# Kernel tuning notes

Hardware: AMD Instinct MI355X
Metric: run time of the kernel (lower is better)

Reference implementation:

```python
import jax, jax.numpy as jnp
import numpy as np

B = 8          # batch_size
N = 2048       # N_particles
D_SP = 2       # spatial dims
D = 16         # D_SP + hidden_dim
K = 32         # max_num_neighbors
R = 0.08       # neighbor_radius
DT = 0.01      # leapfrog step
BIG = 1e9


def setup_inputs() -> dict:
    key = jax.random.key(0)
    ks = jax.random.split(key, 8)
    H, C = 64, 32
    # node state: small random hidden features, deterministic disk positions
    x = jax.random.normal(ks[0], (B * N, D), dtype=jnp.float32) * 0.001
    i = jnp.arange(N, dtype=jnp.float32)
    golden = jnp.pi * (3.0 - jnp.sqrt(5.0))
    theta = i * golden
    r = 0.6 * jnp.sqrt((i + 0.5) / N)
    pos = jnp.stack([r * jnp.cos(theta), r * jnp.sin(theta)], axis=1)  # [N,2]
    pos = jnp.tile(pos, (B, 1)) + 0.01 * jax.random.normal(ks[1], (B * N, 2), dtype=jnp.float32)
    x = x.at[:, :D_SP].set(pos)
    W1 = jax.random.normal(ks[2], (2 * D, H), dtype=jnp.float32) * (1.0 / np.sqrt(2 * D))
    b1 = jnp.zeros((H,), jnp.float32)
    W2 = jax.random.normal(ks[3], (H, C), dtype=jnp.float32) * (1.0 / np.sqrt(H))
    b2 = jnp.zeros((C,), jnp.float32)
    Wout = jax.random.normal(ks[4], (C, 1), dtype=jnp.float32) * (1.0 / np.sqrt(C))
    bout = jnp.zeros((1,), jnp.float32)
    batch = jnp.repeat(jnp.arange(B, dtype=jnp.int64), N)
    return {"x": x, "W1": W1, "b1": b1, "W2": W2, "b2": b2,
            "Wout": Wout, "bout": bout, "batch": batch, "steps": 2}


def reference(x, W1, b1, W2, b2, Wout, bout, batch, steps):
    Bn, Df = x.shape
    Bc = int(np.asarray(batch)[-1]) + 1      # batch is contiguous blocks
    Nn = Bn // Bc
    eye = jnp.eye(Nn, dtype=x.dtype) * BIG   # no self-loops (loop=False)

    def hamiltonian(xv):
        xb = xv.reshape(Bc, Nn, Df)
        pos = xb[:, :, :D_SP]                              # [B,N,2]
        # radius_graph: pairwise sq-dist per simulation, capped at K neighbors
        d2 = jnp.sum((pos[:, :, None, :] - pos[:, None, :, :]) ** 2, axis=-1)  # [B,N,N]
        d2 = d2 + eye
        negd, idx = jax.lax.top_k(-d2, K)                  # K nearest per node
        valid = (-negd) < (R * R)                          # [B,N,K]
        # gather neighbor states (HNNConv message on concat(x_i, x_j))
        xj = xb[jnp.arange(Bc)[:, None, None], idx]        # [B,N,K,D]
        xi = jnp.broadcast_to(xb[:, :, None, :], xj.shape)
        m = jnp.tanh(jnp.concatenate([xi, xj], axis=-1) @ W1 + b1)  # [B,N,K,H]
        m = m @ W2 + b2                                    # [B,N,K,C]
        m = jnp.where(valid[..., None], m, 0.0)
        agg = m.sum(axis=2)                                # sum aggregation [B,N,C]
        h = agg @ Wout + bout                              # per-node Hamiltonian [B,N,1]
        return h.sum()

    for _ in range(int(steps)):
        dHdx = jax.grad(hamiltonian)(x)
        x = x - DT * dHdx
    return x
```

## Files before the change

kernel.cpp:

```cpp
#include <hip/hip_runtime.h>
#include <cstdint>
#include <cstddef>

#define BB   8
#define NN   2048
#define DD   16
#define HHH  64
#define KK   32
#define CAP  96
#define FCAP 48
#define DT_C 0.01f
#define R2_C (0.08f * 0.08f)

#define GRID 17
#define NCEL (GRID * GRID)
#define GOFF 0.68f
#define CINV 12.5f
#define CSTRIDE 320

#define WPB   8
#define BLOCK (WPB * 64)

__device__ __forceinline__ float dist2(float px, float py, float qx, float qy) {
    float dx = __fsub_rn(px, qx);
    float dy = __fsub_rn(py, qy);
    return __fadd_rn(__fmul_rn(dx, dx), __fmul_rn(dy, dy));
}

__device__ __forceinline__ float dtanh_xla(float zz) {
    float xx = fminf(fmaxf(zz, -9.f), 9.f);
    float x2 = xx * xx;
    float p = fmaf(x2, -2.76076847742355e-16f, 2.00018790482477e-13f);
    p = fmaf(x2, p, -8.60467152213735e-11f);
    p = fmaf(x2, p, 5.12229709037114e-08f);
    p = fmaf(x2, p, 1.48572235717979e-05f);
    p = fmaf(x2, p, 6.37261928875436e-04f);
    p = fmaf(x2, p, 4.89352455891786e-03f);
    p = xx * p;
    float q = fmaf(x2, 1.19825839466702e-06f, 1.18534705686654e-04f);
    q = fmaf(x2, q, 2.26843463243900e-03f);
    q = fmaf(x2, q, 4.89352518554385e-03f);
    float r = __builtin_amdgcn_rcpf(q);
    float t = p * r;
    t = fmaf(fmaf(-q, t, p), r, t);
    return fmaf(-t, t, 1.0f);
}

__device__ __forceinline__ int prefix_cnt(unsigned long long m) {
    return (int)__builtin_amdgcn_mbcnt_hi(
        (unsigned)(m >> 32), __builtin_amdgcn_mbcnt_lo((unsigned)m, 0u));
}

__device__ __forceinline__ int swizzled_slot(int blk, int w, int& bbase) {
    bbase = (blk & 7) << 11;
    return (blk >> 3) * WPB + w;
}

__device__ __forceinline__ int clampi(int v, int lo, int hi) {
    return v < lo ? lo : (v > hi ? hi : v);
}

struct Win { int rs0, rl0, rs1, rl1, rs2, rl2, tot; };
__device__ __forceinline__ Win cell_window(const int* CS, float px, float py) {
    Win W;
    int cx = clampi((int)((px + GOFF) * CINV), 0, GRID - 1);
    int cy = clampi((int)((py + GOFF) * CINV), 0, GRID - 1);
    int xlo = cx > 0 ? cx - 1 : 0;
    int xhi = cx < GRID - 1 ? cx + 1 : GRID - 1;
    W.rs0 = 0; W.rl0 = 0; W.rs2 = 0; W.rl2 = 0;
    if (cy > 0) {
        int a = CS[(cy - 1) * GRID + xlo], b = CS[(cy - 1) * GRID + xhi + 1];
        W.rs0 = a; W.rl0 = b - a;
    }
    {
        int a = CS[cy * GRID + xlo], b = CS[cy * GRID + xhi + 1];
        W.rs1 = a; W.rl1 = b - a;
    }
    if (cy < GRID - 1) {
        int a = CS[(cy + 1) * GRID + xlo], b = CS[(cy + 1) * GRID + xhi + 1];
        W.rs2 = a; W.rl2 = b - a;
    }
    W.tot = W.rl0 + W.rl1 + W.rl2;
    return W;
}
__device__ __forceinline__ int win_map(const Win& W, int t) {
    int j = W.rs0 + t;
    int u1 = t - W.rl0;
    if (u1 >= 0) j = W.rs1 + u1;
    int u2 = u1 - W.rl1;
    if (u2 >= 0) j = W.rs2 + u2;
    return j;
}

template <bool FIRST>
__global__ __launch_bounds__(1024) void k_bin(
    const float* __restrict__ x, const float* __restrict__ pos,
    const float* __restrict__ W2, const float* __restrict__ Wout,
    float2* __restrict__ sortedPos, unsigned short* __restrict__ sortedIdx,
    int* __restrict__ cellStart, float* __restrict__ vOut) {
    __shared__ int hist[NCEL], base[NCEL + 1], cursor[NCEL];
    int bat = blockIdx.x, bbase = bat << 11, tid = threadIdx.x;
    if (tid < NCEL) hist[tid] = 0;
    if (blockIdx.x == 0 && tid >= 512 && tid < 512 + HHH) {
        int hh = tid - 512;
        float acc = 0.f;
        for (int c = 0; c < 32; c++) acc = fmaf(W2[hh * 32 + c], Wout[c], acc);
        vOut[hh] = acc;
    }
    __syncthreads();
    float2 q[2]; int cid[2];
#pragma unroll
    for (int u = 0; u < 2; ++u) {
        int i = tid + (u << 10);
        float2 qq = FIRST ? *(const float2*)(x + (size_t)(bbase + i) * DD)
                          : *(const float2*)(pos + (size_t)(bbase + i) * 2);
        q[u] = qq;
        int cx = clampi((int)((qq.x + GOFF) * CINV), 0, GRID - 1);
        int cy = clampi((int)((qq.y + GOFF) * CINV), 0, GRID - 1);
        cid[u] = cy * GRID + cx;
        atomicAdd(&hist[cid[u]], 1);
    }
    __syncthreads();
    if (tid < 64) {
        int loc[5], s = 0;
#pragma unroll
        for (int k = 0; k < 5; ++k) {
            int idx = tid * 5 + k;
            loc[k] = (idx < NCEL) ? hist[idx] : 0;
            s += loc[k];
        }
        int pre = s;
#pragma unroll
        for (int off = 1; off < 64; off <<= 1) {
            int t = __shfl_up(pre, off);
            if (tid >= off) pre += t;
        }
        pre -= s;
#pragma unroll
        for (int k = 0; k < 5; ++k) {
            int idx = tid * 5 + k;
            if (idx <= NCEL) base[idx] = pre;
            pre += loc[k];
        }
    }
    __syncthreads();
    if (tid < NCEL) cursor[tid] = base[tid];
    if (tid <= NCEL) cellStart[bat * CSTRIDE + tid] = base[tid];
    __syncthreads();
#pragma unroll
    for (int u = 0; u < 2; ++u) {
        int dst = atomicAdd(&cursor[cid[u]], 1);
        sortedPos[bbase + dst] = q[u];
        sortedIdx[bbase + dst] = (unsigned short)(tid + (u << 10));
    }
}

__global__ __launch_bounds__(BLOCK, 4) void k_cut(
    const float* __restrict__ x,
    const float2* __restrict__ sortedPos, const unsigned short* __restrict__ sortedIdx,
    const int* __restrict__ cellStart, const float* __restrict__ W1,
    float* __restrict__ cutArr,
    float* __restrict__ Asp, float* __restrict__ Dsp) {
    __shared__ float sD[WPB][CAP];

    int tid = threadIdx.x;
    int w = tid >> 6, lane = tid & 63;
    int bbase;
    int s = swizzled_slot(blockIdx.x, w, bbase);
    int bat = bbase >> 11;
    int gs = bbase + s;

    int jol = (int)sortedIdx[gs];
    const float* xrow = x + (size_t)(bbase + jol) * DD;
    float xv = (lane < DD) ? xrow[lane] : 0.f;
    float px = __shfl(xv, 0), py = __shfl(xv, 1);
    double A = 0.0, Dv = 0.0;
#pragma unroll
    for (int f = 0; f < DD; f++) {
        float xf = __shfl(xv, f);
        A  = fma((double)xf, (double)W1[f * HHH + lane], A);
        Dv = fma((double)xf, (double)W1[(DD + f) * HHH + lane], Dv);
    }
    Asp[((size_t)gs << 6) + lane] = (float)A;
    Dsp[((size_t)gs << 6) + lane] = (float)Dv;

    const int* CS = cellStart + bat * CSTRIDE;
    Win W = cell_window(CS, px, py);
    int cnt = 0;
    for (int c0 = 0; c0 < W.tot; c0 += 64) {
        int t = c0 + lane;
        int j = win_map(W, t);
        bool in = t < W.tot;
        float2 q = sortedPos[bbase + (in ? j : 0)];
        float d2 = dist2(px, py, q.x, q.y);
        bool hit = in && (d2 < R2_C);
        unsigned long long m = __ballot(hit);
        int idx = cnt + prefix_cnt(m);
        if (hit && idx < CAP) sD[w][idx] = d2;
        cnt += (int)__popcll(m);
    }
    if (cnt > CAP) cnt = CAP;
    __threadfence_block();

    float cutoff = R2_C;
    if (cnt > KK + 1) {
        const float INF = 1e30f;
        if (cnt <= 64) {
            float v = (lane < cnt) ? sD[w][lane] : INF;
#pragma unroll
            for (int k = 2; k <= 64; k <<= 1) {
#pragma unroll
                for (int j = k >> 1; j > 0; j >>= 1) {
                    float pv = __shfl_xor(v, j);
                    bool up = ((lane & k) == 0);
                    bool takeMin = (((lane & j) == 0) == up);
                    v = takeMin ? fminf(v, pv) : fmaxf(v, pv);
                }
            }
            cutoff = __shfl(v, KK);
        } else {
            float e0 = (lane < cnt) ? sD[w][lane] : INF;
            float e1 = (lane + 64 < cnt) ? sD[w][lane + 64] : INF;
            int r0 = 0, q0 = 0, r1 = 0, q1 = 0;
            for (int k = 0; k < cnt; k++) {
                float val = sD[w][k];
                r0 += (val < e0); q0 += (val == e0);
                r1 += (val < e1); q1 += (val == e1);
            }
            bool c0 = (r0 <= KK) && (r0 + q0 > KK);
            bool c1 = (r1 <= KK) && (r1 + q1 > KK);
            float cand = c0 ? e0 : (c1 ? e1 : INF);
#pragma unroll
            for (int off = 32; off; off >>= 1) cand = fminf(cand, __shfl_xor(cand, off));
            cutoff = cand;
        }
    }
    if (lane == 0) cutArr[gs] = cutoff;
}

__global__ __launch_bounds__(BLOCK, 4) void k_grad(
    const float* __restrict__ x, const unsigned short* __restrict__ sortedIdx,
    const float2* __restrict__ sortedPos, const int* __restrict__ cellStart,
    const float* __restrict__ cutArr,
    const float* __restrict__ Asp, const float* __restrict__ Dsp,
    const float* __restrict__ W1, const float* __restrict__ b1,
    const float* __restrict__ vArr,
    float* __restrict__ xOut, float* __restrict__ posOut) {
    __shared__ float sW1t[HHH * 33];
    __shared__ alignas(16) unsigned short sFwd[WPB][FCAP];
    __shared__ alignas(16) unsigned short sRev[WPB][CAP];
    __shared__ float sS[WPB][128];

    int tid = threadIdx.x;
    int w = tid >> 6, h = tid & 63;
    int bbase;
    int s = swizzled_slot(blockIdx.x, w, bbase);
    int bat = bbase >> 11;
    int gs = bbase + s;

    for (int t = tid; t < 2 * DD * HHH; t += BLOCK) {
        int f = t >> 6, hh = t & 63;
        sW1t[hh * 33 + f] = W1[t];
    }
    __syncthreads();

    float b1h = b1[h];
    float Apbs = Asp[((size_t)gs << 6) + h] + b1h;
    float Dpbs = Dsp[((size_t)gs << 6) + h] + b1h;
    float vh = vArr[h];

    float2 pp = sortedPos[gs];
    float px = pp.x, py = pp.y;
    float cutp = cutArr[gs];

    const int* CS = cellStart + bat * CSTRIDE;
    Win W = cell_window(CS, px, py);
    int mf = 0, mr = 0;
    for (int c0 = 0; c0 < W.tot; c0 += 64) {
        int t = c0 + h;
        int j = win_map(W, t);
        bool in = t < W.tot;
        int ja = in ? j : 0;
        float2 q = sortedPos[bbase + ja];
        float cutj = cutArr[bbase + ja];
        float d2 = dist2(px, py, q.x, q.y);
        bool hit = in && (d2 < R2_C) && (j != s);
        bool fw = hit && (d2 <= cutp);
        bool rv = hit && (d2 <= cutj);
        unsigned long long mF = __ballot(fw);
        int iF = mf + prefix_cnt(mF);
        if (fw && iF < FCAP) sFwd[w][iF] = (unsigned short)j;
        mf += (int)__popcll(mF);
        unsigned long long mR = __ballot(rv);
        int iR = mr + prefix_cnt(mR);
        if (rv && iR < CAP) sRev[w][iR] = (unsigned short)j;
        mr += (int)__popcll(mR);
    }
    if (mf > FCAP) mf = FCAP;
    if (mr > CAP) mr = CAP;
    __threadfence_block();

    const float* baseD = Dsp + ((size_t)bbase << 6);
    const float* baseA = Asp + ((size_t)bbase << 6);
    double T1 = 0.0, T2 = 0.0;

#define UNPACK8(Q0, Q1, U)                                            \
    unsigned U[8];                                                    \
    U[0] = (unsigned)__builtin_amdgcn_readfirstlane(Q0.x);            \
    U[1] = (unsigned)__builtin_amdgcn_readfirstlane(Q0.y);            \
    U[2] = (unsigned)__builtin_amdgcn_readfirstlane(Q0.z);            \
    U[3] = (unsigned)__builtin_amdgcn_readfirstlane(Q0.w);            \
    U[4] = (unsigned)__builtin_amdgcn_readfirstlane(Q1.x);            \
    U[5] = (unsigned)__builtin_amdgcn_readfirstlane(Q1.y);            \
    U[6] = (unsigned)__builtin_amdgcn_readfirstlane(Q1.z);            \
    U[7] = (unsigned)__builtin_amdgcn_readfirstlane(Q1.w);

    {
        const unsigned short* L = sFwd[w];
        int c = 0;
        for (; c + 16 <= mf; c += 16) {
            int4 q0 = *(const int4*)(L + c);
            int4 q1 = *(const int4*)(L + c + 8);
            UNPACK8(q0, q1, u)
            float d[16];
#pragma unroll
            for (int k = 0; k < 8; ++k) {
                const float* ra = baseD + ((size_t)(u[k] & 0xffffu) << 6);
                const float* rb = baseD + ((size_t)(u[k] >> 16) << 6);
                d[2 * k]     = ra[h];
                d[2 * k + 1] = rb[h];
            }
#pragma unroll
            for (int k = 0; k < 16; ++k) T1 += (double)dtanh_xla(Apbs + d[k]);
        }
        for (; c + 8 <= mf; c += 8) {
            int4 q0 = *(const int4*)(L + c);
            int4 q1 = q0;
            UNPACK8(q0, q1, u)
            float d[8];
#pragma unroll
            for (int k = 0; k < 4; ++k) {
                const float* ra = baseD + ((size_t)(u[k] & 0xffffu) << 6);
                const float* rb = baseD + ((size_t)(u[k] >> 16) << 6);
                d[2 * k]     = ra[h];
                d[2 * k + 1] = rb[h];
            }
#pragma unroll
            for (int k = 0; k < 8; ++k) T1 += (double)dtanh_xla(Apbs + d[k]);
        }
        for (; c < mf; ++c) {
            unsigned jl = (unsigned)__builtin_amdgcn_readfirstlane((int)L[c]);
            T1 += (double)dtanh_xla(Apbs + (baseD + ((size_t)jl << 6))[h]);
        }
    }
    {
        const unsigned short* L = sRev[w];
        int c = 0;
        for (; c + 16 <= mr; c += 16) {
            int4 q0 = *(const int4*)(L + c);
            int4 q1 = *(const int4*)(L + c + 8);
            UNPACK8(q0, q1, u)
            float d[16];
#pragma unroll
            for (int k = 0; k < 8; ++k) {
                const float* ra = baseA + ((size_t)(u[k] & 0xffffu) << 6);
                const float* rb = baseA + ((size_t)(u[k] >> 16) << 6);
                d[2 * k]     = ra[h];
                d[2 * k + 1] = rb[h];
            }
#pragma unroll
            for (int k = 0; k < 16; ++k) T2 += (double)dtanh_xla(Dpbs + d[k]);
        }
        for (; c + 8 <= mr; c += 8) {
            int4 q0 = *(const int4*)(L + c);
            int4 q1 = q0;
            UNPACK8(q0, q1, u)
            float d[8];
#pragma unroll
            for (int k = 0; k < 4; ++k) {
                const float* ra = baseA + ((size_t)(u[k] & 0xffffu) << 6);
                const float* rb = baseA + ((size_t)(u[k] >> 16) << 6);
                d[2 * k]     = ra[h];
                d[2 * k + 1] = rb[h];
            }
#pragma unroll
            for (int k = 0; k < 8; ++k) T2 += (double)dtanh_xla(Dpbs + d[k]);
        }
        for (; c < mr; ++c) {
            unsigned jl = (unsigned)__builtin_amdgcn_readfirstlane((int)L[c]);
            T2 += (double)dtanh_xla(Dpbs + (baseA + ((size_t)jl << 6))[h]);
        }
    }
#undef UNPACK8

    sS[w][h] = vh * (float)T1;
    sS[w][64 + h] = vh * (float)T2;
    __threadfence_block();

    float g;
    {
        int col = h & 31;
        const float* Sv = &sS[w][(col < 16) ? 0 : 64];
        int hh0 = (h < 32) ? 0 : 32;
        double a0 = 0.0, a1 = 0.0, a2 = 0.0, a3 = 0.0;
        for (int hh = hh0; hh < hh0 + 32; hh += 4) {
            a0 = fma((double)sW1t[(hh + 0) * 33 + col], (double)Sv[hh + 0], a0);
            a1 = fma((double)sW1t[(hh + 1) * 33 + col], (double)Sv[hh + 1], a1);
            a2 = fma((double)sW1t[(hh + 2) * 33 + col], (double)Sv[hh + 2], a2);
            a3 = fma((double)sW1t[(hh + 3) * 33 + col], (double)Sv[hh + 3], a3);
        }
        double gd = (a0 + a1) + (a2 + a3);
        double go = __shfl_xor(gd, 32);
        g = (float)(gd + go);
    }
    float g2 = __shfl(g, (h + 16) & 63);
    int jo = (int)sortedIdx[gs];
    if (h < DD) {
        size_t prow = (size_t)(bbase + jo) * DD;
        float xn = __fsub_rn(x[prow + h], __fmul_rn(DT_C, __fadd_rn(g, g2)));
        xOut[prow + h] = xn;
        if (h < 2) posOut[(bbase + jo) * 2 + h] = xn;
    }
}

extern "C" void kernel_launch(void* const* d_in, const int* in_sizes, int n_in,
                              void* d_out, int out_size, void* d_ws, size_t ws_size,
                              hipStream_t stream) {
    const float* x0   = (const float*)d_in[0];
    const float* W1   = (const float*)d_in[1];
    const float* b1   = (const float*)d_in[2];
    const float* W2   = (const float*)d_in[3];
    const float* Wout = (const float*)d_in[5];
    float* out = (float*)d_out;

    float* ws   = (float*)d_ws;
    float* posA = ws;
    float* posB = posA + 32768;
    float* x1   = posB + 32768;
    float* Asp  = x1 + 262144;
    float* Dsp  = Asp + 16384 * 64;
    float* cut  = Dsp + 16384 * 64;
    float2* sPosS = (float2*)(cut + 16384);
    unsigned short* sIdx = (unsigned short*)(sPosS + 16384);
    int* cellStart = (int*)(sIdx + 16384);
    float* vArr = (float*)(cellStart + BB * CSTRIDE);

    const int NB = (BB * NN) / WPB;

    k_bin<true><<<BB, 1024, 0, stream>>>(x0, nullptr, W2, Wout, sPosS, sIdx,
                                         cellStart, vArr);
    k_cut<<<NB, BLOCK, 0, stream>>>(x0, sPosS, sIdx, cellStart, W1, cut, Asp, Dsp);
    k_grad<<<NB, BLOCK, 0, stream>>>(x0, sIdx, sPosS, cellStart, cut, Asp, Dsp,
                                     W1, b1, vArr, x1, posB);
    k_bin<false><<<BB, 1024, 0, stream>>>(nullptr, posB, W2, Wout, sPosS, sIdx,
                                          cellStart, vArr);
    k_cut<<<NB, BLOCK, 0, stream>>>(x1, sPosS, sIdx, cellStart, W1, cut, Asp, Dsp);
    k_grad<<<NB, BLOCK, 0, stream>>>(x1, sIdx, sPosS, cellStart, cut, Asp, Dsp,
                                     W1, b1, vArr, out, posA);
}
```

Baseline: 189.1 us.

## Split fp64 accumulators, prefetch first two neighbor chunks, halve waves per block

Splits the fp64 projection accumulation into four independent chains per output to shorten the dependency chain. Peels the first two 64-wide chunks of the cell-window scan in both kernels so their position and cutoff loads are issued before any ballot processing, hiding load latency. Also reduces warps per block from 8 to 4. The split accumulators reorder the summation, which can change rounding slightly, and the extra live registers may lower occupancy.

```diff
diff --git a/kernel.cpp b/kernel.cpp
--- a/kernel.cpp
+++ b/kernel.cpp
@@ -18,7 +18,7 @@
 #define CINV 12.5f
 #define CSTRIDE 320
 
-#define WPB   8
+#define WPB   4
 #define BLOCK (WPB * 64)
 
 __device__ __forceinline__ float dist2(float px, float py, float qx, float qy) {
@@ -174,30 +174,64 @@
     const float* xrow = x + (size_t)(bbase + jol) * DD;
     float xv = (lane < DD) ? xrow[lane] : 0.f;
     float px = __shfl(xv, 0), py = __shfl(xv, 1);
-    double A = 0.0, Dv = 0.0;
-#pragma unroll
-    for (int f = 0; f < DD; f++) {
-        float xf = __shfl(xv, f);
-        A  = fma((double)xf, (double)W1[f * HHH + lane], A);
-        Dv = fma((double)xf, (double)W1[(DD + f) * HHH + lane], Dv);
-    }
-    Asp[((size_t)gs << 6) + lane] = (float)A;
-    Dsp[((size_t)gs << 6) + lane] = (float)Dv;
+    double A0 = 0.0, A1 = 0.0, A2 = 0.0, A3 = 0.0;
+    double D0 = 0.0, D1 = 0.0, D2v = 0.0, D3 = 0.0;
+#pragma unroll
+    for (int f = 0; f < DD; f += 4) {
+        float xf0 = __shfl(xv, f),     xf1 = __shfl(xv, f + 1);
+        float xf2 = __shfl(xv, f + 2), xf3 = __shfl(xv, f + 3);
+        A0 = fma((double)xf0, (double)W1[(f + 0) * HHH + lane], A0);
+        A1 = fma((double)xf1, (double)W1[(f + 1) * HHH + lane], A1);
+        A2 = fma((double)xf2, (double)W1[(f + 2) * HHH + lane], A2);
+        A3 = fma((double)xf3, (double)W1[(f + 3) * HHH + lane], A3);
+        D0 = fma((double)xf0, (double)W1[(DD + f + 0) * HHH + lane], D0);
+        D1 = fma((double)xf1, (double)W1[(DD + f + 1) * HHH + lane], D1);
+        D2v = fma((double)xf2, (double)W1[(DD + f + 2) * HHH + lane], D2v);
+        D3 = fma((double)xf3, (double)W1[(DD + f + 3) * HHH + lane], D3);
+    }
+    Asp[((size_t)gs << 6) + lane] = (float)((A0 + A1) + (A2 + A3));
+    Dsp[((size_t)gs << 6) + lane] = (float)((D0 + D1) + (D2v + D3));
 
     const int* CS = cellStart + bat * CSTRIDE;
     Win W = cell_window(CS, px, py);
     int cnt = 0;
-    for (int c0 = 0; c0 < W.tot; c0 += 64) {
-        int t = c0 + lane;
-        int j = win_map(W, t);
-        bool in = t < W.tot;
-        float2 q = sortedPos[bbase + (in ? j : 0)];
-        float d2 = dist2(px, py, q.x, q.y);
-        bool hit = in && (d2 < R2_C);
+    {
+        int t0 = lane, t1 = 64 + lane;
+        bool in0 = t0 < W.tot, in1 = t1 < W.tot;
+        int ja0 = in0 ? win_map(W, t0) : 0;
+        float2 q0 = sortedPos[bbase + ja0];
+        float2 q1;
+        bool have1 = W.tot > 64;
+        if (have1) {
+            int ja1 = in1 ? win_map(W, t1) : 0;
+            q1 = sortedPos[bbase + ja1];
+        }
+        float d2 = dist2(px, py, q0.x, q0.y);
+        bool hit = in0 && (d2 < R2_C);
         unsigned long long m = __ballot(hit);
         int idx = cnt + prefix_cnt(m);
         if (hit && idx < CAP) sD[w][idx] = d2;
         cnt += (int)__popcll(m);
+        if (have1) {
+            float e2 = dist2(px, py, q1.x, q1.y);
+            bool h2 = in1 && (e2 < R2_C);
+            unsigned long long m2 = __ballot(h2);
+            int i2 = cnt + prefix_cnt(m2);
+            if (h2 && i2 < CAP) sD[w][i2] = e2;
+            cnt += (int)__popcll(m2);
+        }
+        for (int c0 = 128; c0 < W.tot; c0 += 64) {
+            int t = c0 + lane;
+            int j = win_map(W, t);
+            bool in = t < W.tot;
+            float2 q = sortedPos[bbase + (in ? j : 0)];
+            float dd = dist2(px, py, q.x, q.y);
+            bool ht = in && (dd < R2_C);
+            unsigned long long mm = __ballot(ht);
+            int ix = cnt + prefix_cnt(mm);
+            if (ht && ix < CAP) sD[w][ix] = dd;
+            cnt += (int)__popcll(mm);
+        }
     }
     if (cnt > CAP) cnt = CAP;
     __threadfence_block();
@@ -276,26 +310,49 @@
     const int* CS = cellStart + bat * CSTRIDE;
     Win W = cell_window(CS, px, py);
     int mf = 0, mr = 0;
-    for (int c0 = 0; c0 < W.tot; c0 += 64) {
-        int t = c0 + h;
-        int j = win_map(W, t);
-        bool in = t < W.tot;
-        int ja = in ? j : 0;
-        float2 q = sortedPos[bbase + ja];
-        float cutj = cutArr[bbase + ja];
-        float d2 = dist2(px, py, q.x, q.y);
-        bool hit = in && (d2 < R2_C) && (j != s);
-        bool fw = hit && (d2 <= cutp);
-        bool rv = hit && (d2 <= cutj);
-        unsigned long long mF = __ballot(fw);
-        int iF = mf + prefix_cnt(mF);
-        if (fw && iF < FCAP) sFwd[w][iF] = (unsigned short)j;
-        mf += (int)__popcll(mF);
-        unsigned long long mR = __ballot(rv);
-        int iR = mr + prefix_cnt(mR);
-        if (rv && iR < CAP) sRev[w][iR] = (unsigned short)j;
-        mr += (int)__popcll(mR);
-    }
+#define PROC(IN, J, Q, CUTJ)                                              \
+    {                                                                     \
+        float d2 = dist2(px, py, (Q).x, (Q).y);                           \
+        bool hit = (IN) && (d2 < R2_C) && ((J) != s);                     \
+        bool fw = hit && (d2 <= cutp);                                    \
+        bool rv = hit && (d2 <= (CUTJ));                                  \
+        unsigned long long mF = __ballot(fw);                             \
+        int iF = mf + prefix_cnt(mF);                                     \
+        if (fw && iF < FCAP) sFwd[w][iF] = (unsigned short)(J);           \
+        mf += (int)__popcll(mF);                                          \
+        unsigned long long mR = __ballot(rv);                             \
+        int iR = mr + prefix_cnt(mR);                                     \
+        if (rv && iR < CAP) sRev[w][iR] = (unsigned short)(J);            \
+        mr += (int)__popcll(mR);                                          \
+    }
+    {
+        int t0 = h, t1 = 64 + h;
+        bool in0 = t0 < W.tot, in1 = t1 < W.tot;
+        int j0 = win_map(W, t0);
+        int ja0 = in0 ? j0 : 0;
+        float2 q0 = sortedPos[bbase + ja0];
+        float cut0 = cutArr[bbase + ja0];
+        bool have1 = W.tot > 64;
+        int j1 = 0; float2 q1; float cut1 = 0.f;
+        if (have1) {
+            j1 = win_map(W, t1);
+            int ja1 = in1 ? j1 : 0;
+            q1 = sortedPos[bbase + ja1];
+            cut1 = cutArr[bbase + ja1];
+        }
+        PROC(in0, j0, q0, cut0)
+        if (have1) PROC(in1, j1, q1, cut1)
+        for (int c0 = 128; c0 < W.tot; c0 += 64) {
+            int t = c0 + h;
+            int j = win_map(W, t);
+            bool in = t < W.tot;
+            int ja = in ? j : 0;
+            float2 q = sortedPos[bbase + ja];
+            float cutj = cutArr[bbase + ja];
+            PROC(in, j, q, cutj)
+        }
+    }
+#undef PROC
     if (mf > FCAP) mf = FCAP;
     if (mr > CAP) mr = CAP;
     __threadfence_block();
```

New measurement: 190.0 us. About the same (+0.5%).
